# Kernel tuning notes

Measured on AMD Instinct MI355X. Metric: run time of the kernel, lower is better.

Reference implementation:

```python
import jax, jax.numpy as jnp
import numpy as np

DIM_Q = 512
DIM_K = 512
DIM_V = 512
NUM_HEADS = 8
TEMPERATURE = 0.1
LN_EPS = 1e-5


def setup_inputs() -> dict:
    key = jax.random.key(0)
    ks = jax.random.split(key, 12)
    B, n_q, n_k = 8, 1024, 1024
    s = 0.02
    return {
        "Q": jax.random.normal(ks[0], (B, n_q, DIM_Q), jnp.float32),
        "K": jax.random.normal(ks[1], (B, n_k, DIM_K), jnp.float32),
        "mask": jnp.ones((B, n_k), dtype=bool),
        "Wq": jax.random.normal(ks[2], (DIM_Q, DIM_V), jnp.float32) * s,
        "bq": jnp.zeros((DIM_V,), jnp.float32),
        "Wk": jax.random.normal(ks[3], (DIM_K, DIM_V), jnp.float32) * s,
        "bk": jnp.zeros((DIM_V,), jnp.float32),
        "Wv": jax.random.normal(ks[4], (DIM_K, DIM_V), jnp.float32) * s,
        "bv": jnp.zeros((DIM_V,), jnp.float32),
        "Wo": jax.random.normal(ks[5], (DIM_V, DIM_V), jnp.float32) * s,
        "bo": jnp.zeros((DIM_V,), jnp.float32),
        "gamma": jnp.ones((DIM_V,), jnp.float32),
        "beta": jnp.zeros((DIM_V,), jnp.float32),
    }


def _mab(Q, K, mask, Wq, bq, Wk, bk, Wv, bv, Wo, bo, gamma, beta):
    B, n_q, _ = Q.shape
    n_k = K.shape[1]
    H = NUM_HEADS
    d_head = DIM_V // H
    # projections, split heads: [B, H, n, d_head]
    Qh = (Q @ Wq + bq).reshape(B, n_q, H, d_head).transpose(0, 2, 1, 3)
    Kh = (K @ Wk + bk).reshape(B, n_k, H, d_head).transpose(0, 2, 1, 3)
    Vh = (K @ Wv + bv).reshape(B, n_k, H, d_head).transpose(0, 2, 1, 3)
    scale = 1.0 / (np.sqrt(d_head) * TEMPERATURE)
    A = jnp.einsum("bhqd,bhkd->bhqk", Qh, Kh) * scale
    A = jnp.where(mask[:, None, None, :], A, -jnp.inf)
    A = jax.nn.softmax(A, axis=-1)
    O = jnp.einsum("bhqk,bhkd->bhqd", A, Vh)
    O = O.transpose(0, 2, 1, 3).reshape(B, n_q, DIM_V)
    # fused output FFN + residual + LN
    O = O + jax.nn.relu(O @ Wo + bo)
    mu = jnp.mean(O, axis=-1, keepdims=True)
    var = jnp.var(O, axis=-1, keepdims=True)
    return (O - mu) * jax.lax.rsqrt(var + LN_EPS) * gamma + beta


def reference(Q, K, mask, Wq, bq, Wk, bk, Wv, bv, Wo, bo, gamma, beta):
    return _mab(Q, K, mask, Wq, bq, Wk, bk, Wv, bv, Wo, bo, gamma, beta)
```

## Files before the change

### kernel.cpp

```cpp
#include <hip/hip_runtime.h>

typedef __bf16 bf16;
typedef bf16 bf16x4 __attribute__((ext_vector_type(4)));
typedef bf16 bf16x8 __attribute__((ext_vector_type(8)));
typedef float floatx4 __attribute__((ext_vector_type(4)));

#define NB 8
#define NQ 1024
#define NK 1024
#define DIM 512
#define NH 8
#define DH 64

__device__ __forceinline__ void async16(const void* g, void* l) {
    __builtin_amdgcn_global_load_lds(
        (const __attribute__((address_space(1))) unsigned int*)(unsigned long long)(g),
        (__attribute__((address_space(3))) unsigned int*)(unsigned long long)(l),
        16, 0, 0);
}

__global__ __launch_bounds__(256) void prep_fused(
    const float* __restrict__ Q, const float* __restrict__ K,
    const float* __restrict__ Wq, const float* __restrict__ Wk,
    const float* __restrict__ Wv, const float* __restrict__ Wo,
    bf16* __restrict__ Qb, bf16* __restrict__ Kb, bf16* __restrict__ Wt)
{
    __shared__ bf16 Tl[64][68];
    const int bid = blockIdx.x;
    if (bid < 4096) {
        const int i = bid * 256 + threadIdx.x;
        float4 a = ((const float4*)Q)[i];
        float4 c = ((const float4*)K)[i];
        bf16x4 qa = {(bf16)a.x, (bf16)a.y, (bf16)a.z, (bf16)a.w};
        bf16x4 ka = {(bf16)c.x, (bf16)c.y, (bf16)c.z, (bf16)c.w};
        *(bf16x4*)(Qb + (size_t)i * 4) = qa;
        *(bf16x4*)(Kb + (size_t)i * 4) = ka;
    } else {
        const int bid2 = bid - 4096;
        const int w = bid2 >> 6;
        const int bx = bid2 & 7, by = (bid2 >> 3) & 7;
        const float* W = (w == 0) ? Wq : (w == 1) ? Wk : (w == 2) ? Wv : Wo;
        bf16* out = Wt + (size_t)w * DIM * DIM;
        const int k0 = bx * 64, n0 = by * 64;
        const int tx = threadIdx.x & 15, ty = threadIdx.x >> 4;
        for (int pass = 0; pass < 4; ++pass) {
            int k = ty + pass * 16;
            float4 v = *(const float4*)&W[(size_t)(k0 + k) * DIM + n0 + tx * 4];
            Tl[tx * 4 + 0][k] = (bf16)v.x;
            Tl[tx * 4 + 1][k] = (bf16)v.y;
            Tl[tx * 4 + 2][k] = (bf16)v.z;
            Tl[tx * 4 + 3][k] = (bf16)v.w;
        }
        __syncthreads();
        for (int pass = 0; pass < 4; ++pass) {
            int n = ty + pass * 16;
            bf16x4 ov = *(const bf16x4*)&Tl[n][tx * 4];
            *(bf16x4*)&out[(size_t)(n0 + n) * DIM + k0 + tx * 4] = ov;
        }
    }
}

__global__ __launch_bounds__(256) void proj_fused(
    const bf16* __restrict__ Qb, const bf16* __restrict__ Kb,
    const bf16* __restrict__ Wt,
    const float* __restrict__ bq, const float* __restrict__ bk,
    const float* __restrict__ bv,
    bf16* __restrict__ Qp, bf16* __restrict__ Kp, bf16* __restrict__ Vpt)
{
    __shared__ __attribute__((aligned(16))) bf16 sh[16384];
    bf16* As = sh;
    bf16* Bs = sh + 8192;
    const int t = threadIdx.x;
    const int wave = t >> 6, lane = t & 63, quad = lane >> 4, l16 = lane & 15;
    const int wr = wave >> 1, wc = wave & 1;
    const int bid = blockIdx.x;
    const bool isQ = bid < 256;
    const bf16* A; const bf16* W; int m0, n0;
    if (isQ) { A = Qb; W = Wt;             m0 = (bid >> 2) * 128;  n0 = (bid & 3) * 128; }
    else     { int b2 = bid - 256;
               A = Kb; W = Wt + 512 * DIM; m0 = (b2 >> 3) * 128;   n0 = (b2 & 7) * 128; }

    const int r1 = t >> 3, s1 = t & 7;
    const int p1 = s1 ^ (r1 & 7);
    const bf16* aSrc = A + (size_t)(m0 + r1) * DIM + p1 * 8;
    const bf16* wSrc = W + (size_t)(n0 + r1) * DIM + p1 * 8;

    floatx4 acc[4][4];
    for (int i = 0; i < 4; ++i)
        for (int j = 0; j < 4; ++j) acc[i][j] = (floatx4){0.f, 0.f, 0.f, 0.f};

    for (int kt = 0; kt < 8; ++kt) {
        __syncthreads();
        const int ko = kt * 64;
        #pragma unroll
        for (int j = 0; j < 4; ++j) {
            async16(aSrc + ko + (size_t)j * 32 * DIM, As + (t + j * 256) * 8);
            async16(wSrc + ko + (size_t)j * 32 * DIM, Bs + (t + j * 256) * 8);
        }
        __syncthreads();
        #pragma unroll
        for (int ks = 0; ks < 2; ++ks) {
            bf16x8 af[4], bfr[4];
            #pragma unroll
            for (int mi = 0; mi < 4; ++mi) {
                const int row = wr * 64 + mi * 16 + l16;
                af[mi] = *(const bf16x8*)(As + row * 64 + (((ks * 4 + quad) ^ (row & 7)) << 3));
            }
            #pragma unroll
            for (int ni = 0; ni < 4; ++ni) {
                const int row = wc * 64 + ni * 16 + l16;
                bfr[ni] = *(const bf16x8*)(Bs + row * 64 + (((ks * 4 + quad) ^ (row & 7)) << 3));
            }
            #pragma unroll
            for (int mi = 0; mi < 4; ++mi)
                #pragma unroll
                for (int ni = 0; ni < 4; ++ni)
                    acc[mi][ni] = __builtin_amdgcn_mfma_f32_16x16x32_bf16(
                        af[mi], bfr[ni], acc[mi][ni], 0, 0, 0);
        }
    }

    const bool isV = (!isQ) && (n0 >= 512);
    if (!isV) {
        bf16* out = isQ ? Qp : Kp;
        const float* bias = isQ ? bq : bk;
        for (int ni = 0; ni < 4; ++ni) {
            const int n = n0 + wc * 64 + ni * 16 + l16;
            const float bb = bias[n];
            const int hd = n >> 6, d = n & 63;
            for (int mi = 0; mi < 4; ++mi) {
                for (int r = 0; r < 4; ++r) {
                    const int m = m0 + wr * 64 + mi * 16 + quad * 4 + r;
                    const int b = m >> 10, q = m & 1023;
                    out[((size_t)(b * 8 + hd) * 1024 + q) * 64 + d] = (bf16)(acc[mi][ni][r] + bb);
                }
            }
        }
    } else {
        __syncthreads();
        for (int ni = 0; ni < 4; ++ni) {
            const int n = wc * 64 + ni * 16 + l16;
            const float bb = bv[n0 + n - 512];
            for (int mi = 0; mi < 4; ++mi) {
                const int mb = wr * 64 + mi * 16 + quad * 4;
                const int slot = ((mb >> 3) ^ (n & 15));
                bf16x4 pk = {(bf16)(acc[mi][ni][0] + bb), (bf16)(acc[mi][ni][1] + bb),
                             (bf16)(acc[mi][ni][2] + bb), (bf16)(acc[mi][ni][3] + bb)};
                *(bf16x4*)(sh + n * 128 + slot * 8 + (mb & 7)) = pk;
            }
        }
        __syncthreads();
        const int n = t >> 1, hf = t & 1;
        const int nv = n0 + n - 512, hd = nv >> 6, d = nv & 63;
        const int b = m0 >> 10, qb = m0 & 1023;
        bf16* dst = Vpt + ((size_t)(b * 8 + hd) * 64 + d) * 1024 + qb + hf * 64;
        #pragma unroll
        for (int j = 0; j < 8; ++j) {
            const int ch = hf * 8 + j;
            const int slot = ch ^ (n & 15);
            bf16x8 v8 = *(const bf16x8*)(sh + n * 128 + slot * 8);
            *(bf16x8*)(dst + j * 8) = v8;
        }
    }
}

__global__ __launch_bounds__(256) void attn_kernel(
    const bf16* __restrict__ Qp, const bf16* __restrict__ Kp,
    const bf16* __restrict__ Vpt, const int* __restrict__ mask,
    bf16* __restrict__ Oa)
{
    const int bh = blockIdx.x & 63, qblk = blockIdx.x >> 6;
    const int b = bh >> 3, hd = bh & 7;
    const int t = threadIdx.x;
    const int wave = t >> 6, lane = t & 63, quad = lane >> 4, l16 = lane & 15;
    const float scale = 1.25f;

    __shared__ __attribute__((aligned(16))) bf16 Kt[64 * 64];
    __shared__ __attribute__((aligned(16))) bf16 Vt[64 * 64];
    __shared__ __attribute__((aligned(16))) bf16 Pl[4][32][72];

    const bf16* Qbase = Qp + ((size_t)bh * NQ + qblk * 128 + wave * 32) * DH;
    const bf16* Kbase = Kp + (size_t)bh * NK * DH;
    const bf16* Vbase = Vpt + (size_t)bh * DH * NK;
    const int* mrow = mask + b * NK;

    bf16x8 qf[2][2];
    for (int g = 0; g < 2; ++g)
        for (int hh = 0; hh < 2; ++hh)
            qf[g][hh] = *(const bf16x8*)(Qbase + (g * 16 + l16) * DH + hh * 32 + quad * 8);

    floatx4 o[2][4];
    float lsum[2];
    for (int g = 0; g < 2; ++g) {
        lsum[g] = 0.f;
        for (int i = 0; i < 4; ++i) o[g][i] = (floatx4){0.f, 0.f, 0.f, 0.f};
    }

    const int r1 = t >> 3, s1 = t & 7;
    const int p1 = s1 ^ (r1 & 7);
    const bf16* kSrc = Kbase + r1 * 64 + p1 * 8;
    const bf16* vSrc = Vbase + (size_t)r1 * 1024 + p1 * 8;
    bf16* kDst0 = Kt + t * 8;
    bf16* kDst1 = Kt + (t + 256) * 8;
    bf16* vDst0 = Vt + t * 8;
    bf16* vDst1 = Vt + (t + 256) * 8;

    for (int kt = 0; kt < NK / 64; ++kt) {
        __syncthreads();
        async16(kSrc + kt * 4096, kDst0);
        async16(kSrc + kt * 4096 + 32 * 64, kDst1);
        async16(vSrc + kt * 64, vDst0);
        async16(vSrc + kt * 64 + (size_t)32 * 1024, vDst1);
        __syncthreads();

        bf16x8 kb[4][2];
        #pragma unroll
        for (int sub = 0; sub < 4; ++sub) {
            const int rowk = sub * 16 + l16;
            kb[sub][0] = *(const bf16x8*)(Kt + rowk * 64 + ((quad ^ (rowk & 7)) << 3));
            kb[sub][1] = *(const bf16x8*)(Kt + rowk * 64 + (((quad + 4) ^ (rowk & 7)) << 3));
        }
        floatx4 sf[2][4];
        #pragma unroll
        for (int g = 0; g < 2; ++g)
            #pragma unroll
            for (int sub = 0; sub < 4; ++sub) {
                floatx4 s = {0.f, 0.f, 0.f, 0.f};
                s = __builtin_amdgcn_mfma_f32_16x16x32_bf16(kb[sub][0], qf[g][0], s, 0, 0, 0);
                s = __builtin_amdgcn_mfma_f32_16x16x32_bf16(kb[sub][1], qf[g][1], s, 0, 0, 0);
                sf[g][sub] = s;
            }
        #pragma unroll
        for (int sub = 0; sub < 4; ++sub) {
            const int4 m4 = *(const int4*)&mrow[kt * 64 + sub * 16 + quad * 4];
            const float md0 = m4.x ? 0.f : -3.0e38f;
            const float md1 = m4.y ? 0.f : -3.0e38f;
            const float md2 = m4.z ? 0.f : -3.0e38f;
            const float md3 = m4.w ? 0.f : -3.0e38f;
            #pragma unroll
            for (int g = 0; g < 2; ++g) {
                float p0 = __expf(sf[g][sub][0] * scale + md0);
                float p1v = __expf(sf[g][sub][1] * scale + md1);
                float p2 = __expf(sf[g][sub][2] * scale + md2);
                float p3 = __expf(sf[g][sub][3] * scale + md3);
                sf[g][sub][0] = p0; sf[g][sub][1] = p1v;
                sf[g][sub][2] = p2; sf[g][sub][3] = p3;
                lsum[g] += p0 + p1v + p2 + p3;
            }
        }
        #pragma unroll
        for (int g = 0; g < 2; ++g)
            #pragma unroll
            for (int sub = 0; sub < 4; ++sub) {
                bf16x4 pk = {(bf16)sf[g][sub][0], (bf16)sf[g][sub][1],
                             (bf16)sf[g][sub][2], (bf16)sf[g][sub][3]};
                *(bf16x4*)&Pl[wave][g * 16 + l16][sub * 16 + quad * 4] = pk;
            }
        bf16x8 af[2][2];
        for (int g = 0; g < 2; ++g)
            for (int hh = 0; hh < 2; ++hh)
                af[g][hh] = *(const bf16x8*)&Pl[wave][g * 16 + l16][hh * 32 + quad * 8];
        #pragma unroll
        for (int dsub = 0; dsub < 4; ++dsub) {
            const int rowd = dsub * 16 + l16;
            bf16x8 v0 = *(const bf16x8*)(Vt + rowd * 64 + ((quad ^ (rowd & 7)) << 3));
            bf16x8 v1 = *(const bf16x8*)(Vt + rowd * 64 + (((quad + 4) ^ (rowd & 7)) << 3));
            #pragma unroll
            for (int g = 0; g < 2; ++g) {
                o[g][dsub] = __builtin_amdgcn_mfma_f32_16x16x32_bf16(af[g][0], v0, o[g][dsub], 0, 0, 0);
                o[g][dsub] = __builtin_amdgcn_mfma_f32_16x16x32_bf16(af[g][1], v1, o[g][dsub], 0, 0, 0);
            }
        }
    }

    for (int g = 0; g < 2; ++g) {
        float lr = lsum[g];
        lr += __shfl_xor(lr, 16, 64);
        lr += __shfl_xor(lr, 32, 64);
        const float inv = 1.f / lr;
        float linv[4];
        for (int r = 0; r < 4; ++r) linv[r] = __shfl(inv, quad * 4 + r, 64);
        for (int dsub = 0; dsub < 4; ++dsub) {
            for (int r = 0; r < 4; ++r) {
                const int q = qblk * 128 + wave * 32 + g * 16 + quad * 4 + r;
                const int col = hd * 64 + dsub * 16 + l16;
                Oa[((size_t)(b * NQ + q)) * DIM + col] = (bf16)(o[g][dsub][r] * linv[r]);
            }
        }
    }
}

__global__ __launch_bounds__(256) void ffn_gemm(
    const bf16* __restrict__ Oa, const bf16* __restrict__ W,
    const float* __restrict__ bias, float* __restrict__ Y)
{
    __shared__ __attribute__((aligned(16))) bf16 As[64 * 64];
    __shared__ __attribute__((aligned(16))) bf16 Bs[128 * 64];
    const int t = threadIdx.x;
    const int wave = t >> 6, lane = t & 63, quad = lane >> 4, l16 = lane & 15;
    const int wr = wave >> 1, wc = wave & 1;
    const int m0 = (blockIdx.x >> 2) * 64, n0 = (blockIdx.x & 3) * 128;

    const int r1 = t >> 3, s1 = t & 7;
    const int p1 = s1 ^ (r1 & 7);
    const bf16* aSrc = Oa + (size_t)(m0 + r1) * DIM + p1 * 8;
    const bf16* wSrc = W  + (size_t)(n0 + r1) * DIM + p1 * 8;

    floatx4 acc[2][4];
    for (int i = 0; i < 2; ++i)
        for (int j = 0; j < 4; ++j) acc[i][j] = (floatx4){0.f, 0.f, 0.f, 0.f};

    for (int kt = 0; kt < 8; ++kt) {
        __syncthreads();
        const int ko = kt * 64;
        async16(aSrc + ko, As + t * 8);
        async16(aSrc + ko + (size_t)32 * DIM, As + (t + 256) * 8);
        #pragma unroll
        for (int j = 0; j < 4; ++j)
            async16(wSrc + ko + (size_t)j * 32 * DIM, Bs + (t + j * 256) * 8);
        __syncthreads();
        #pragma unroll
        for (int ks = 0; ks < 2; ++ks) {
            bf16x8 af[2], bfr[4];
            #pragma unroll
            for (int mi = 0; mi < 2; ++mi) {
                const int row = wr * 32 + mi * 16 + l16;
                af[mi] = *(const bf16x8*)(As + row * 64 + (((ks * 4 + quad) ^ (row & 7)) << 3));
            }
            #pragma unroll
            for (int ni = 0; ni < 4; ++ni) {
                const int row = wc * 64 + ni * 16 + l16;
                bfr[ni] = *(const bf16x8*)(Bs + row * 64 + (((ks * 4 + quad) ^ (row & 7)) << 3));
            }
            #pragma unroll
            for (int mi = 0; mi < 2; ++mi)
                #pragma unroll
                for (int ni = 0; ni < 4; ++ni)
                    acc[mi][ni] = __builtin_amdgcn_mfma_f32_16x16x32_bf16(
                        af[mi], bfr[ni], acc[mi][ni], 0, 0, 0);
        }
    }

    for (int ni = 0; ni < 4; ++ni) {
        const int n = n0 + wc * 64 + ni * 16 + l16;
        const float bb = bias[n];
        for (int mi = 0; mi < 2; ++mi) {
            for (int r = 0; r < 4; ++r) {
                const int m = m0 + wr * 32 + mi * 16 + quad * 4 + r;
                const float ov = (float)Oa[(size_t)m * DIM + n];
                const float v = acc[mi][ni][r] + bb;
                Y[(size_t)m * DIM + n] = ov + fmaxf(v, 0.f);
            }
        }
    }
}

__global__ __launch_bounds__(256) void ln_kernel(
    const float* __restrict__ Y, const float* __restrict__ gamma,
    const float* __restrict__ beta, float* __restrict__ out)
{
    const int row  = blockIdx.x * 4 + (threadIdx.x >> 6);
    const int lane = threadIdx.x & 63;
    const float* y = Y + (size_t)row * DIM;
    float4 a = ((const float4*)y)[lane];
    float4 c = ((const float4*)y)[lane + 64];
    float s  = a.x + a.y + a.z + a.w + c.x + c.y + c.z + c.w;
    float sq = a.x*a.x + a.y*a.y + a.z*a.z + a.w*a.w
             + c.x*c.x + c.y*c.y + c.z*c.z + c.w*c.w;
    for (int mk = 32; mk >= 1; mk >>= 1) {
        s  += __shfl_xor(s,  mk, 64);
        sq += __shfl_xor(sq, mk, 64);
    }
    const float mu  = s * (1.f / 512.f);
    const float var = sq * (1.f / 512.f) - mu * mu;
    const float inv = rsqrtf(var + 1e-5f);
    float4 g1 = ((const float4*)gamma)[lane];
    float4 g2 = ((const float4*)gamma)[lane + 64];
    float4 b1 = ((const float4*)beta)[lane];
    float4 b2 = ((const float4*)beta)[lane + 64];
    float4 o1, o2;
    o1.x = (a.x - mu) * inv * g1.x + b1.x;
    o1.y = (a.y - mu) * inv * g1.y + b1.y;
    o1.z = (a.z - mu) * inv * g1.z + b1.z;
    o1.w = (a.w - mu) * inv * g1.w + b1.w;
    o2.x = (c.x - mu) * inv * g2.x + b2.x;
    o2.y = (c.y - mu) * inv * g2.y + b2.y;
    o2.z = (c.z - mu) * inv * g2.z + b2.z;
    o2.w = (c.w - mu) * inv * g2.w + b2.w;
    float* orow = out + (size_t)row * DIM;
    ((float4*)orow)[lane]      = o1;
    ((float4*)orow)[lane + 64] = o2;
}

extern "C" void kernel_launch(void* const* d_in, const int* in_sizes, int n_in,
                              void* d_out, int out_size, void* d_ws, size_t ws_size,
                              hipStream_t stream) {
    const float* Q  = (const float*)d_in[0];
    const float* K  = (const float*)d_in[1];
    const int*   mask = (const int*)d_in[2];
    const float* Wq = (const float*)d_in[3];
    const float* bq = (const float*)d_in[4];
    const float* Wk = (const float*)d_in[5];
    const float* bk = (const float*)d_in[6];
    const float* Wv = (const float*)d_in[7];
    const float* bv = (const float*)d_in[8];
    const float* Wo = (const float*)d_in[9];
    const float* bo = (const float*)d_in[10];
    const float* gamma = (const float*)d_in[11];
    const float* beta  = (const float*)d_in[12];

    char* ws = (char*)d_ws;
    bf16* Wt  = (bf16*)(ws);
    bf16* Qb  = (bf16*)(ws + 2097152);
    bf16* Kb  = (bf16*)(ws + 10485760);
    bf16* Qp  = (bf16*)(ws + 18874368);
    bf16* Kp  = (bf16*)(ws + 27262976);
    bf16* Vpt = (bf16*)(ws + 35651584);
    bf16* Oa  = (bf16*)(ws + 44040192);
    float* Yf = (float*)(ws + 52428800);
    float* out = (float*)d_out;

    prep_fused<<<4352, 256, 0, stream>>>(Q, K, Wq, Wk, Wv, Wo, Qb, Kb, Wt);
    proj_fused<<<768, 256, 0, stream>>>(Qb, Kb, Wt, bq, bk, bv, Qp, Kp, Vpt);
    attn_kernel<<<512, 256, 0, stream>>>(Qp, Kp, Vpt, mask, Oa);
    ffn_gemm<<<512, 256, 0, stream>>>(Oa, Wt + 3 * 262144, bo, Yf);
    ln_kernel<<<2048, 256, 0, stream>>>(Yf, gamma, beta, out);
}
```

Before: 189.9 us.

## Fuse FFN GEMM with LayerNorm, shrink attention tiles, reorder projection blocks

The FFN GEMM, residual, ReLU and LayerNorm now run in one kernel. Each block owns 32 full rows, keeps the Oa tile resident in LDS for the residual, and reduces row statistics across waves, so the fp32 intermediate Y no longer makes a round trip through memory. The attention kernel now gives each wave 16 query rows instead of 32 and launches twice as many blocks. It also uses exp2 with a prescaled constant and a swizzled P buffer in LDS. The projection kernel's block-to-tile mapping is transposed so that consecutive blocks share a weight tile. In exchange, the FFN kernel launches only 256 blocks with a large LDS footprint, and smaller attention tiles reload K/V more often per query.

```diff
diff --git a/kernel.cpp b/kernel.cpp
--- a/kernel.cpp
+++ b/kernel.cpp
@@ -76,9 +76,9 @@
     const int bid = blockIdx.x;
     const bool isQ = bid < 256;
     const bf16* A; const bf16* W; int m0, n0;
-    if (isQ) { A = Qb; W = Wt;             m0 = (bid >> 2) * 128;  n0 = (bid & 3) * 128; }
+    if (isQ) { A = Qb; W = Wt;             m0 = (bid & 63) * 128;  n0 = (bid >> 6) * 128; }
     else     { int b2 = bid - 256;
-               A = Kb; W = Wt + 512 * DIM; m0 = (b2 >> 3) * 128;   n0 = (b2 & 7) * 128; }
+               A = Kb; W = Wt + 512 * DIM; m0 = (b2 & 63) * 128;   n0 = (b2 >> 6) * 128; }
 
     const int r1 = t >> 3, s1 = t & 7;
     const int p1 = s1 ^ (r1 & 7);
@@ -173,28 +173,24 @@
     const int b = bh >> 3, hd = bh & 7;
     const int t = threadIdx.x;
     const int wave = t >> 6, lane = t & 63, quad = lane >> 4, l16 = lane & 15;
-    const float scale = 1.25f;
+    const float scale2 = 1.8033688011112042f;
 
     __shared__ __attribute__((aligned(16))) bf16 Kt[64 * 64];
     __shared__ __attribute__((aligned(16))) bf16 Vt[64 * 64];
-    __shared__ __attribute__((aligned(16))) bf16 Pl[4][32][72];
-
-    const bf16* Qbase = Qp + ((size_t)bh * NQ + qblk * 128 + wave * 32) * DH;
+    __shared__ __attribute__((aligned(16))) bf16 Pl[4][16 * 64];
+
+    const bf16* Qbase = Qp + ((size_t)bh * NQ + qblk * 64 + wave * 16) * DH;
     const bf16* Kbase = Kp + (size_t)bh * NK * DH;
     const bf16* Vbase = Vpt + (size_t)bh * DH * NK;
     const int* mrow = mask + b * NK;
 
-    bf16x8 qf[2][2];
-    for (int g = 0; g < 2; ++g)
-        for (int hh = 0; hh < 2; ++hh)
-            qf[g][hh] = *(const bf16x8*)(Qbase + (g * 16 + l16) * DH + hh * 32 + quad * 8);
-
-    floatx4 o[2][4];
-    float lsum[2];
-    for (int g = 0; g < 2; ++g) {
-        lsum[g] = 0.f;
-        for (int i = 0; i < 4; ++i) o[g][i] = (floatx4){0.f, 0.f, 0.f, 0.f};
-    }
+    bf16x8 qf[2];
+    for (int hh = 0; hh < 2; ++hh)
+        qf[hh] = *(const bf16x8*)(Qbase + l16 * DH + hh * 32 + quad * 8);
+
+    floatx4 o[4];
+    float lsum = 0.f;
+    for (int i = 0; i < 4; ++i) o[i] = (floatx4){0.f, 0.f, 0.f, 0.f};
 
     const int r1 = t >> 3, s1 = t & 7;
     const int p1 = s1 ^ (r1 & 7);
@@ -220,16 +216,14 @@
             kb[sub][0] = *(const bf16x8*)(Kt + rowk * 64 + ((quad ^ (rowk & 7)) << 3));
             kb[sub][1] = *(const bf16x8*)(Kt + rowk * 64 + (((quad + 4) ^ (rowk & 7)) << 3));
         }
-        floatx4 sf[2][4];
-        #pragma unroll
-        for (int g = 0; g < 2; ++g)
-            #pragma unroll
-            for (int sub = 0; sub < 4; ++sub) {
-                floatx4 s = {0.f, 0.f, 0.f, 0.f};
-                s = __builtin_amdgcn_mfma_f32_16x16x32_bf16(kb[sub][0], qf[g][0], s, 0, 0, 0);
-                s = __builtin_amdgcn_mfma_f32_16x16x32_bf16(kb[sub][1], qf[g][1], s, 0, 0, 0);
-                sf[g][sub] = s;
-            }
+        floatx4 sf[4];
+        #pragma unroll
+        for (int sub = 0; sub < 4; ++sub) {
+            floatx4 s = {0.f, 0.f, 0.f, 0.f};
+            s = __builtin_amdgcn_mfma_f32_16x16x32_bf16(kb[sub][0], qf[0], s, 0, 0, 0);
+            s = __builtin_amdgcn_mfma_f32_16x16x32_bf16(kb[sub][1], qf[1], s, 0, 0, 0);
+            sf[sub] = s;
+        }
         #pragma unroll
         for (int sub = 0; sub < 4; ++sub) {
             const int4 m4 = *(const int4*)&mrow[kt * 64 + sub * 16 + quad * 4];
@@ -237,159 +231,177 @@
             const float md1 = m4.y ? 0.f : -3.0e38f;
             const float md2 = m4.z ? 0.f : -3.0e38f;
             const float md3 = m4.w ? 0.f : -3.0e38f;
-            #pragma unroll
-            for (int g = 0; g < 2; ++g) {
-                float p0 = __expf(sf[g][sub][0] * scale + md0);
-                float p1v = __expf(sf[g][sub][1] * scale + md1);
-                float p2 = __expf(sf[g][sub][2] * scale + md2);
-                float p3 = __expf(sf[g][sub][3] * scale + md3);
-                sf[g][sub][0] = p0; sf[g][sub][1] = p1v;
-                sf[g][sub][2] = p2; sf[g][sub][3] = p3;
-                lsum[g] += p0 + p1v + p2 + p3;
-            }
-        }
-        #pragma unroll
-        for (int g = 0; g < 2; ++g)
-            #pragma unroll
-            for (int sub = 0; sub < 4; ++sub) {
-                bf16x4 pk = {(bf16)sf[g][sub][0], (bf16)sf[g][sub][1],
-                             (bf16)sf[g][sub][2], (bf16)sf[g][sub][3]};
-                *(bf16x4*)&Pl[wave][g * 16 + l16][sub * 16 + quad * 4] = pk;
-            }
-        bf16x8 af[2][2];
-        for (int g = 0; g < 2; ++g)
-            for (int hh = 0; hh < 2; ++hh)
-                af[g][hh] = *(const bf16x8*)&Pl[wave][g * 16 + l16][hh * 32 + quad * 8];
+            float p0 = exp2f(fmaf(sf[sub][0], scale2, md0));
+            float p1v = exp2f(fmaf(sf[sub][1], scale2, md1));
+            float p2 = exp2f(fmaf(sf[sub][2], scale2, md2));
+            float p3 = exp2f(fmaf(sf[sub][3], scale2, md3));
+            sf[sub][0] = p0; sf[sub][1] = p1v; sf[sub][2] = p2; sf[sub][3] = p3;
+            lsum += p0 + p1v + p2 + p3;
+        }
+        #pragma unroll
+        for (int sub = 0; sub < 4; ++sub) {
+            bf16x4 pk = {(bf16)sf[sub][0], (bf16)sf[sub][1],
+                         (bf16)sf[sub][2], (bf16)sf[sub][3]};
+            const int p = sub * 2 + (quad >> 1);
+            const int slot = p ^ (l16 & 7);
+            *(bf16x4*)&Pl[wave][l16 * 64 + slot * 8 + (quad & 1) * 4] = pk;
+        }
+        bf16x8 af[2];
+        #pragma unroll
+        for (int hh = 0; hh < 2; ++hh) {
+            const int p = hh * 4 + quad;
+            const int slot = p ^ (l16 & 7);
+            af[hh] = *(const bf16x8*)&Pl[wave][l16 * 64 + slot * 8];
+        }
         #pragma unroll
         for (int dsub = 0; dsub < 4; ++dsub) {
             const int rowd = dsub * 16 + l16;
             bf16x8 v0 = *(const bf16x8*)(Vt + rowd * 64 + ((quad ^ (rowd & 7)) << 3));
             bf16x8 v1 = *(const bf16x8*)(Vt + rowd * 64 + (((quad + 4) ^ (rowd & 7)) << 3));
-            #pragma unroll
-            for (int g = 0; g < 2; ++g) {
-                o[g][dsub] = __builtin_amdgcn_mfma_f32_16x16x32_bf16(af[g][0], v0, o[g][dsub], 0, 0, 0);
-                o[g][dsub] = __builtin_amdgcn_mfma_f32_16x16x32_bf16(af[g][1], v1, o[g][dsub], 0, 0, 0);
-            }
-        }
-    }
-
-    for (int g = 0; g < 2; ++g) {
-        float lr = lsum[g];
-        lr += __shfl_xor(lr, 16, 64);
-        lr += __shfl_xor(lr, 32, 64);
-        const float inv = 1.f / lr;
-        float linv[4];
-        for (int r = 0; r < 4; ++r) linv[r] = __shfl(inv, quad * 4 + r, 64);
-        for (int dsub = 0; dsub < 4; ++dsub) {
-            for (int r = 0; r < 4; ++r) {
-                const int q = qblk * 128 + wave * 32 + g * 16 + quad * 4 + r;
-                const int col = hd * 64 + dsub * 16 + l16;
-                Oa[((size_t)(b * NQ + q)) * DIM + col] = (bf16)(o[g][dsub][r] * linv[r]);
-            }
-        }
-    }
-}
-
-__global__ __launch_bounds__(256) void ffn_gemm(
+            o[dsub] = __builtin_amdgcn_mfma_f32_16x16x32_bf16(af[0], v0, o[dsub], 0, 0, 0);
+            o[dsub] = __builtin_amdgcn_mfma_f32_16x16x32_bf16(af[1], v1, o[dsub], 0, 0, 0);
+        }
+    }
+
+    float lr = lsum;
+    lr += __shfl_xor(lr, 16, 64);
+    lr += __shfl_xor(lr, 32, 64);
+    const float inv = 1.f / lr;
+    float linv[4];
+    for (int r = 0; r < 4; ++r) linv[r] = __shfl(inv, quad * 4 + r, 64);
+    for (int dsub = 0; dsub < 4; ++dsub) {
+        for (int r = 0; r < 4; ++r) {
+            const int q = qblk * 64 + wave * 16 + quad * 4 + r;
+            const int col = hd * 64 + dsub * 16 + l16;
+            Oa[((size_t)(b * NQ + q)) * DIM + col] = (bf16)(o[dsub][r] * linv[r]);
+        }
+    }
+}
+
+__global__ __launch_bounds__(256) void ffn_ln(
     const bf16* __restrict__ Oa, const bf16* __restrict__ W,
-    const float* __restrict__ bias, float* __restrict__ Y)
+    const float* __restrict__ bo, const float* __restrict__ gamma,
+    const float* __restrict__ beta, float* __restrict__ out)
 {
-    __shared__ __attribute__((aligned(16))) bf16 As[64 * 64];
-    __shared__ __attribute__((aligned(16))) bf16 Bs[128 * 64];
+    __shared__ __attribute__((aligned(16))) bf16 As[32 * 512];
+    __shared__ __attribute__((aligned(16))) bf16 Bs[512 * 32];
     const int t = threadIdx.x;
     const int wave = t >> 6, lane = t & 63, quad = lane >> 4, l16 = lane & 15;
-    const int wr = wave >> 1, wc = wave & 1;
-    const int m0 = (blockIdx.x >> 2) * 64, n0 = (blockIdx.x & 3) * 128;
-
-    const int r1 = t >> 3, s1 = t & 7;
-    const int p1 = s1 ^ (r1 & 7);
-    const bf16* aSrc = Oa + (size_t)(m0 + r1) * DIM + p1 * 8;
-    const bf16* wSrc = W  + (size_t)(n0 + r1) * DIM + p1 * 8;
-
-    floatx4 acc[2][4];
+    const int m0 = blockIdx.x * 32;
+
+    #pragma unroll
+    for (int j = 0; j < 8; ++j) {
+        const int c = t + j * 256;
+        const int row = c >> 6, slot = c & 63;
+        const int p = (slot & 56) | ((slot & 7) ^ (row & 7));
+        async16(Oa + (size_t)(m0 + row) * DIM + p * 8, As + row * 512 + slot * 8);
+    }
+
+    floatx4 acc[2][8];
     for (int i = 0; i < 2; ++i)
-        for (int j = 0; j < 4; ++j) acc[i][j] = (floatx4){0.f, 0.f, 0.f, 0.f};
-
-    for (int kt = 0; kt < 8; ++kt) {
-        __syncthreads();
-        const int ko = kt * 64;
-        async16(aSrc + ko, As + t * 8);
-        async16(aSrc + ko + (size_t)32 * DIM, As + (t + 256) * 8);
-        #pragma unroll
-        for (int j = 0; j < 4; ++j)
-            async16(wSrc + ko + (size_t)j * 32 * DIM, Bs + (t + j * 256) * 8);
-        __syncthreads();
-        #pragma unroll
-        for (int ks = 0; ks < 2; ++ks) {
-            bf16x8 af[2], bfr[4];
-            #pragma unroll
-            for (int mi = 0; mi < 2; ++mi) {
-                const int row = wr * 32 + mi * 16 + l16;
-                af[mi] = *(const bf16x8*)(As + row * 64 + (((ks * 4 + quad) ^ (row & 7)) << 3));
-            }
-            #pragma unroll
-            for (int ni = 0; ni < 4; ++ni) {
-                const int row = wc * 64 + ni * 16 + l16;
-                bfr[ni] = *(const bf16x8*)(Bs + row * 64 + (((ks * 4 + quad) ^ (row & 7)) << 3));
-            }
-            #pragma unroll
-            for (int mi = 0; mi < 2; ++mi)
-                #pragma unroll
-                for (int ni = 0; ni < 4; ++ni)
-                    acc[mi][ni] = __builtin_amdgcn_mfma_f32_16x16x32_bf16(
-                        af[mi], bfr[ni], acc[mi][ni], 0, 0, 0);
-        }
-    }
-
-    for (int ni = 0; ni < 4; ++ni) {
-        const int n = n0 + wc * 64 + ni * 16 + l16;
-        const float bb = bias[n];
+        for (int j = 0; j < 8; ++j) acc[i][j] = (floatx4){0.f, 0.f, 0.f, 0.f};
+
+    for (int kt = 0; kt < 16; ++kt) {
+        __syncthreads();
+        #pragma unroll
+        for (int j = 0; j < 8; ++j) {
+            const int c = t + j * 256;
+            const int n = c >> 2, slot = c & 3;
+            const int p = slot ^ ((n >> 1) & 3);
+            async16(W + (size_t)n * DIM + kt * 32 + p * 8, Bs + n * 32 + slot * 8);
+        }
+        __syncthreads();
+        bf16x8 af[2], bfr[8];
+        #pragma unroll
         for (int mi = 0; mi < 2; ++mi) {
+            const int row = mi * 16 + l16;
+            const int part = kt * 4 + quad;
+            const int slot = (part & 56) | ((part & 7) ^ (row & 7));
+            af[mi] = *(const bf16x8*)(As + row * 512 + slot * 8);
+        }
+        #pragma unroll
+        for (int ni = 0; ni < 8; ++ni) {
+            const int n = wave * 128 + ni * 16 + l16;
+            const int slot = quad ^ ((n >> 1) & 3);
+            bfr[ni] = *(const bf16x8*)(Bs + n * 32 + slot * 8);
+        }
+        #pragma unroll
+        for (int mi = 0; mi < 2; ++mi)
+            #pragma unroll
+            for (int ni = 0; ni < 8; ++ni)
+                acc[mi][ni] = __builtin_amdgcn_mfma_f32_16x16x32_bf16(
+                    af[mi], bfr[ni], acc[mi][ni], 0, 0, 0);
+    }
+
+    #pragma unroll
+    for (int ni = 0; ni < 8; ++ni) {
+        const int n = wave * 128 + ni * 16 + l16;
+        const float bb = bo[n];
+        const int part = n >> 3, noff = n & 7;
+        #pragma unroll
+        for (int mi = 0; mi < 2; ++mi) {
+            #pragma unroll
             for (int r = 0; r < 4; ++r) {
-                const int m = m0 + wr * 32 + mi * 16 + quad * 4 + r;
-                const float ov = (float)Oa[(size_t)m * DIM + n];
-                const float v = acc[mi][ni][r] + bb;
-                Y[(size_t)m * DIM + n] = ov + fmaxf(v, 0.f);
-            }
-        }
-    }
-}
-
-__global__ __launch_bounds__(256) void ln_kernel(
-    const float* __restrict__ Y, const float* __restrict__ gamma,
-    const float* __restrict__ beta, float* __restrict__ out)
-{
-    const int row  = blockIdx.x * 4 + (threadIdx.x >> 6);
-    const int lane = threadIdx.x & 63;
-    const float* y = Y + (size_t)row * DIM;
-    float4 a = ((const float4*)y)[lane];
-    float4 c = ((const float4*)y)[lane + 64];
-    float s  = a.x + a.y + a.z + a.w + c.x + c.y + c.z + c.w;
-    float sq = a.x*a.x + a.y*a.y + a.z*a.z + a.w*a.w
-             + c.x*c.x + c.y*c.y + c.z*c.z + c.w*c.w;
-    for (int mk = 32; mk >= 1; mk >>= 1) {
-        s  += __shfl_xor(s,  mk, 64);
-        sq += __shfl_xor(sq, mk, 64);
-    }
-    const float mu  = s * (1.f / 512.f);
-    const float var = sq * (1.f / 512.f) - mu * mu;
-    const float inv = rsqrtf(var + 1e-5f);
-    float4 g1 = ((const float4*)gamma)[lane];
-    float4 g2 = ((const float4*)gamma)[lane + 64];
-    float4 b1 = ((const float4*)beta)[lane];
-    float4 b2 = ((const float4*)beta)[lane + 64];
-    float4 o1, o2;
-    o1.x = (a.x - mu) * inv * g1.x + b1.x;
-    o1.y = (a.y - mu) * inv * g1.y + b1.y;
-    o1.z = (a.z - mu) * inv * g1.z + b1.z;
-    o1.w = (a.w - mu) * inv * g1.w + b1.w;
-    o2.x = (c.x - mu) * inv * g2.x + b2.x;
-    o2.y = (c.y - mu) * inv * g2.y + b2.y;
-    o2.z = (c.z - mu) * inv * g2.z + b2.z;
-    o2.w = (c.w - mu) * inv * g2.w + b2.w;
-    float* orow = out + (size_t)row * DIM;
-    ((float4*)orow)[lane]      = o1;
-    ((float4*)orow)[lane + 64] = o2;
+                const int row = mi * 16 + quad * 4 + r;
+                const int slot = (part & 56) | ((part & 7) ^ (row & 7));
+                const float res = (float)As[row * 512 + slot * 8 + noff];
+                acc[mi][ni][r] = res + fmaxf(acc[mi][ni][r] + bb, 0.f);
+            }
+        }
+    }
+
+    __syncthreads();
+    float* Sm  = (float*)Bs;
+    float* Sq  = Sm + 128;
+    float* Mu  = Sm + 256;
+    float* Inv = Sm + 288;
+    #pragma unroll
+    for (int mi = 0; mi < 2; ++mi) {
+        #pragma unroll
+        for (int r = 0; r < 4; ++r) {
+            float s = 0.f, q2 = 0.f;
+            #pragma unroll
+            for (int ni = 0; ni < 8; ++ni) {
+                const float v = acc[mi][ni][r];
+                s += v; q2 += v * v;
+            }
+            s  += __shfl_xor(s, 1, 64);  q2 += __shfl_xor(q2, 1, 64);
+            s  += __shfl_xor(s, 2, 64);  q2 += __shfl_xor(q2, 2, 64);
+            s  += __shfl_xor(s, 4, 64);  q2 += __shfl_xor(q2, 4, 64);
+            s  += __shfl_xor(s, 8, 64);  q2 += __shfl_xor(q2, 8, 64);
+            if (l16 == 0) {
+                const int row = mi * 16 + quad * 4 + r;
+                Sm[wave * 32 + row] = s;
+                Sq[wave * 32 + row] = q2;
+            }
+        }
+    }
+    __syncthreads();
+    if (t < 32) {
+        const float s  = Sm[t] + Sm[32 + t] + Sm[64 + t] + Sm[96 + t];
+        const float q2 = Sq[t] + Sq[32 + t] + Sq[64 + t] + Sq[96 + t];
+        const float mu = s * (1.f / 512.f);
+        const float var = q2 * (1.f / 512.f) - mu * mu;
+        Mu[t] = mu;
+        Inv[t] = rsqrtf(var + 1e-5f);
+    }
+    __syncthreads();
+
+    #pragma unroll
+    for (int ni = 0; ni < 8; ++ni) {
+        const int n = wave * 128 + ni * 16 + l16;
+        const float gv = gamma[n], btv = beta[n];
+        #pragma unroll
+        for (int mi = 0; mi < 2; ++mi) {
+            #pragma unroll
+            for (int r = 0; r < 4; ++r) {
+                const int row = mi * 16 + quad * 4 + r;
+                const float mu = Mu[row], iv = Inv[row];
+                out[(size_t)(m0 + row) * DIM + n] =
+                    (acc[mi][ni][r] - mu) * iv * gv + btv;
+            }
+        }
+    }
 }
 
 extern "C" void kernel_launch(void* const* d_in, const int* in_sizes, int n_in,
@@ -417,12 +429,10 @@
     bf16* Kp  = (bf16*)(ws + 27262976);
     bf16* Vpt = (bf16*)(ws + 35651584);
     bf16* Oa  = (bf16*)(ws + 44040192);
-    float* Yf = (float*)(ws + 52428800);
     float* out = (float*)d_out;
 
     prep_fused<<<4352, 256, 0, stream>>>(Q, K, Wq, Wk, Wv, Wo, Qb, Kb, Wt);
     proj_fused<<<768, 256, 0, stream>>>(Qb, Kb, Wt, bq, bk, bv, Qp, Kp, Vpt);
-    attn_kernel<<<512, 256, 0, stream>>>(Qp, Kp, Vpt, mask, Oa);
-    ffn_gemm<<<512, 256, 0, stream>>>(Oa, Wt + 3 * 262144, bo, Yf);
-    ln_kernel<<<2048, 256, 0, stream>>>(Yf, gamma, beta, out);
-}
+    attn_kernel<<<1024, 256, 0, stream>>>(Qp, Kp, Vpt, mask, Oa);
+    ffn_ln<<<256, 256, 0, stream>>>(Oa, Wt + 3 * 262144, bo, gamma, beta, out);
+}
```

Result: no change. 186.9 us (-1.6%).

## Double-buffer attention K/V tiles, swizzle P scratch, enlarge FFN tiles, reorder block mapping

Applied to the files above, without the earlier changes.

The attention kernel now double-buffers its K and V tiles, issuing the async loads for the next tile before computing on the current one. The prefetch is meant to overlap global-to-LDS transfer with the MFMA work and drops one barrier per iteration. The padded P scratch becomes an XOR-swizzled 64-wide layout to avoid LDS bank conflicts. The FFN GEMM moves to 128x128 tiles on half as many blocks, and the projection and FFN block indices are remapped so neighbouring blocks share the same weight columns. Risks are that a single barrier may not reliably order the async LDS writes against reads, that the extra LDS lowers occupancy, and that halving the FFN grid underfills the GPU.

```diff
diff --git a/kernel.cpp b/kernel.cpp
--- a/kernel.cpp
+++ b/kernel.cpp
@@ -76,9 +76,9 @@
     const int bid = blockIdx.x;
     const bool isQ = bid < 256;
     const bf16* A; const bf16* W; int m0, n0;
-    if (isQ) { A = Qb; W = Wt;             m0 = (bid >> 2) * 128;  n0 = (bid & 3) * 128; }
+    if (isQ) { A = Qb; W = Wt;             m0 = (bid & 63) * 128;  n0 = (bid >> 6) * 128; }
     else     { int b2 = bid - 256;
-               A = Kb; W = Wt + 512 * DIM; m0 = (b2 >> 3) * 128;   n0 = (b2 & 7) * 128; }
+               A = Kb; W = Wt + 512 * DIM; m0 = (b2 & 63) * 128;   n0 = (b2 >> 6) * 128; }
 
     const int r1 = t >> 3, s1 = t & 7;
     const int p1 = s1 ^ (r1 & 7);
@@ -175,9 +175,9 @@
     const int wave = t >> 6, lane = t & 63, quad = lane >> 4, l16 = lane & 15;
     const float scale = 1.25f;
 
-    __shared__ __attribute__((aligned(16))) bf16 Kt[64 * 64];
-    __shared__ __attribute__((aligned(16))) bf16 Vt[64 * 64];
-    __shared__ __attribute__((aligned(16))) bf16 Pl[4][32][72];
+    __shared__ __attribute__((aligned(16))) bf16 Kt[2][64 * 64];
+    __shared__ __attribute__((aligned(16))) bf16 Vt[2][64 * 64];
+    __shared__ __attribute__((aligned(16))) bf16 Pl[4][32 * 64];
 
     const bf16* Qbase = Qp + ((size_t)bh * NQ + qblk * 128 + wave * 32) * DH;
     const bf16* Kbase = Kp + (size_t)bh * NK * DH;
@@ -200,25 +200,29 @@
     const int p1 = s1 ^ (r1 & 7);
     const bf16* kSrc = Kbase + r1 * 64 + p1 * 8;
     const bf16* vSrc = Vbase + (size_t)r1 * 1024 + p1 * 8;
-    bf16* kDst0 = Kt + t * 8;
-    bf16* kDst1 = Kt + (t + 256) * 8;
-    bf16* vDst0 = Vt + t * 8;
-    bf16* vDst1 = Vt + (t + 256) * 8;
+
+    async16(kSrc, Kt[0] + t * 8);
+    async16(kSrc + 32 * 64, Kt[0] + (t + 256) * 8);
+    async16(vSrc, Vt[0] + t * 8);
+    async16(vSrc + (size_t)32 * 1024, Vt[0] + (t + 256) * 8);
 
     for (int kt = 0; kt < NK / 64; ++kt) {
         __syncthreads();
-        async16(kSrc + kt * 4096, kDst0);
-        async16(kSrc + kt * 4096 + 32 * 64, kDst1);
-        async16(vSrc + kt * 64, vDst0);
-        async16(vSrc + kt * 64 + (size_t)32 * 1024, vDst1);
-        __syncthreads();
+        const int cur = kt & 1;
+        if (kt < NK / 64 - 1) {
+            const int nxt = 1 - cur;
+            async16(kSrc + (kt + 1) * 4096, Kt[nxt] + t * 8);
+            async16(kSrc + (kt + 1) * 4096 + 32 * 64, Kt[nxt] + (t + 256) * 8);
+            async16(vSrc + (kt + 1) * 64, Vt[nxt] + t * 8);
+            async16(vSrc + (kt + 1) * 64 + (size_t)32 * 1024, Vt[nxt] + (t + 256) * 8);
+        }
 
         bf16x8 kb[4][2];
         #pragma unroll
         for (int sub = 0; sub < 4; ++sub) {
             const int rowk = sub * 16 + l16;
-            kb[sub][0] = *(const bf16x8*)(Kt + rowk * 64 + ((quad ^ (rowk & 7)) << 3));
-            kb[sub][1] = *(const bf16x8*)(Kt + rowk * 64 + (((quad + 4) ^ (rowk & 7)) << 3));
+            kb[sub][0] = *(const bf16x8*)(Kt[cur] + rowk * 64 + ((quad ^ (rowk & 7)) << 3));
+            kb[sub][1] = *(const bf16x8*)(Kt[cur] + rowk * 64 + (((quad + 4) ^ (rowk & 7)) << 3));
         }
         floatx4 sf[2][4];
         #pragma unroll
@@ -254,17 +258,22 @@
             for (int sub = 0; sub < 4; ++sub) {
                 bf16x4 pk = {(bf16)sf[g][sub][0], (bf16)sf[g][sub][1],
                              (bf16)sf[g][sub][2], (bf16)sf[g][sub][3]};
-                *(bf16x4*)&Pl[wave][g * 16 + l16][sub * 16 + quad * 4] = pk;
+                const int slot = (sub * 2 + (quad >> 1)) ^ (l16 & 7);
+                *(bf16x4*)&Pl[wave][(g * 16 + l16) * 64 + slot * 8 + (quad & 1) * 4] = pk;
             }
         bf16x8 af[2][2];
+        #pragma unroll
         for (int g = 0; g < 2; ++g)
-            for (int hh = 0; hh < 2; ++hh)
-                af[g][hh] = *(const bf16x8*)&Pl[wave][g * 16 + l16][hh * 32 + quad * 8];
+            #pragma unroll
+            for (int hh = 0; hh < 2; ++hh) {
+                const int slot = (hh * 4 + quad) ^ (l16 & 7);
+                af[g][hh] = *(const bf16x8*)&Pl[wave][(g * 16 + l16) * 64 + slot * 8];
+            }
         #pragma unroll
         for (int dsub = 0; dsub < 4; ++dsub) {
             const int rowd = dsub * 16 + l16;
-            bf16x8 v0 = *(const bf16x8*)(Vt + rowd * 64 + ((quad ^ (rowd & 7)) << 3));
-            bf16x8 v1 = *(const bf16x8*)(Vt + rowd * 64 + (((quad + 4) ^ (rowd & 7)) << 3));
+            bf16x8 v0 = *(const bf16x8*)(Vt[cur] + rowd * 64 + ((quad ^ (rowd & 7)) << 3));
+            bf16x8 v1 = *(const bf16x8*)(Vt[cur] + rowd * 64 + (((quad + 4) ^ (rowd & 7)) << 3));
             #pragma unroll
             for (int g = 0; g < 2; ++g) {
                 o[g][dsub] = __builtin_amdgcn_mfma_f32_16x16x32_bf16(af[g][0], v0, o[g][dsub], 0, 0, 0);
@@ -292,39 +301,39 @@
 
 __global__ __launch_bounds__(256) void ffn_gemm(
     const bf16* __restrict__ Oa, const bf16* __restrict__ W,
-    const float* __restrict__ bias, float* __restrict__ Y)
+    const float* __restrict__ bias, float* __restrict__ Yf)
 {
-    __shared__ __attribute__((aligned(16))) bf16 As[64 * 64];
+    __shared__ __attribute__((aligned(16))) bf16 As[128 * 64];
     __shared__ __attribute__((aligned(16))) bf16 Bs[128 * 64];
     const int t = threadIdx.x;
     const int wave = t >> 6, lane = t & 63, quad = lane >> 4, l16 = lane & 15;
     const int wr = wave >> 1, wc = wave & 1;
-    const int m0 = (blockIdx.x >> 2) * 64, n0 = (blockIdx.x & 3) * 128;
+    const int m0 = (blockIdx.x & 63) * 128, n0 = (blockIdx.x >> 6) * 128;
 
     const int r1 = t >> 3, s1 = t & 7;
     const int p1 = s1 ^ (r1 & 7);
     const bf16* aSrc = Oa + (size_t)(m0 + r1) * DIM + p1 * 8;
     const bf16* wSrc = W  + (size_t)(n0 + r1) * DIM + p1 * 8;
 
-    floatx4 acc[2][4];
-    for (int i = 0; i < 2; ++i)
+    floatx4 acc[4][4];
+    for (int i = 0; i < 4; ++i)
         for (int j = 0; j < 4; ++j) acc[i][j] = (floatx4){0.f, 0.f, 0.f, 0.f};
 
     for (int kt = 0; kt < 8; ++kt) {
         __syncthreads();
         const int ko = kt * 64;
-        async16(aSrc + ko, As + t * 8);
-        async16(aSrc + ko + (size_t)32 * DIM, As + (t + 256) * 8);
-        #pragma unroll
-        for (int j = 0; j < 4; ++j)
+        #pragma unroll
+        for (int j = 0; j < 4; ++j) {
+            async16(aSrc + ko + (size_t)j * 32 * DIM, As + (t + j * 256) * 8);
             async16(wSrc + ko + (size_t)j * 32 * DIM, Bs + (t + j * 256) * 8);
+        }
         __syncthreads();
         #pragma unroll
         for (int ks = 0; ks < 2; ++ks) {
-            bf16x8 af[2], bfr[4];
-            #pragma unroll
-            for (int mi = 0; mi < 2; ++mi) {
-                const int row = wr * 32 + mi * 16 + l16;
+            bf16x8 af[4], bfr[4];
+            #pragma unroll
+            for (int mi = 0; mi < 4; ++mi) {
+                const int row = wr * 64 + mi * 16 + l16;
                 af[mi] = *(const bf16x8*)(As + row * 64 + (((ks * 4 + quad) ^ (row & 7)) << 3));
             }
             #pragma unroll
@@ -333,7 +342,7 @@
                 bfr[ni] = *(const bf16x8*)(Bs + row * 64 + (((ks * 4 + quad) ^ (row & 7)) << 3));
             }
             #pragma unroll
-            for (int mi = 0; mi < 2; ++mi)
+            for (int mi = 0; mi < 4; ++mi)
                 #pragma unroll
                 for (int ni = 0; ni < 4; ++ni)
                     acc[mi][ni] = __builtin_amdgcn_mfma_f32_16x16x32_bf16(
@@ -344,12 +353,11 @@
     for (int ni = 0; ni < 4; ++ni) {
         const int n = n0 + wc * 64 + ni * 16 + l16;
         const float bb = bias[n];
-        for (int mi = 0; mi < 2; ++mi) {
+        for (int mi = 0; mi < 4; ++mi) {
             for (int r = 0; r < 4; ++r) {
-                const int m = m0 + wr * 32 + mi * 16 + quad * 4 + r;
+                const int m = m0 + wr * 64 + mi * 16 + quad * 4 + r;
                 const float ov = (float)Oa[(size_t)m * DIM + n];
-                const float v = acc[mi][ni][r] + bb;
-                Y[(size_t)m * DIM + n] = ov + fmaxf(v, 0.f);
+                Yf[(size_t)m * DIM + n] = ov + fmaxf(acc[mi][ni][r] + bb, 0.f);
             }
         }
     }
@@ -423,6 +431,6 @@
     prep_fused<<<4352, 256, 0, stream>>>(Q, K, Wq, Wk, Wv, Wo, Qb, Kb, Wt);
     proj_fused<<<768, 256, 0, stream>>>(Qb, Kb, Wt, bq, bk, bv, Qp, Kp, Vpt);
     attn_kernel<<<512, 256, 0, stream>>>(Qp, Kp, Vpt, mask, Oa);
-    ffn_gemm<<<512, 256, 0, stream>>>(Oa, Wt + 3 * 262144, bo, Yf);
+    ffn_gemm<<<256, 256, 0, stream>>>(Oa, Wt + 3 * 262144, bo, Yf);
     ln_kernel<<<2048, 256, 0, stream>>>(Yf, gamma, beta, out);
 }
```

New measurement: 178.2 us. -6.2%, faster.
